# Performance work log

Hardware: AMD Instinct MI355X
Metric: run time of the kernel (lower is better)

Reference implementation:

```python
import jax, jax.numpy as jnp
import numpy as np
import math

D_MODEL = 1024
HEADS = 16
HEAD_DIM = D_MODEL // HEADS
FFN = 4096
B, S = 2, 2048


def _layer_norm(x, gamma, beta, eps=1e-5):
    mean = jnp.mean(x, axis=-1, keepdims=True)
    var = jnp.mean((x - mean) ** 2, axis=-1, keepdims=True)
    return gamma * (x - mean) / jnp.sqrt(var + eps) + beta


def _sdpa(q, k, v, mask):
    # q,k,v: [B,H,S,dh]; mask: [S,S] additive, broadcasts over B,H
    scaled = jnp.einsum('bhqd,bhkd->bhqk', q, k) / math.sqrt(q.shape[-1])
    scaled = scaled + mask
    attn = jax.nn.softmax(scaled, axis=-1)
    return jnp.einsum('bhqk,bhkd->bhqd', attn, v)


def setup_inputs() -> dict:
    key = jax.random.key(0)
    ks = jax.random.split(key, 12)
    s = 0.02
    inp = {
        'x': jax.random.normal(ks[0], (B, S, D_MODEL), jnp.float32),
        'y': jax.random.normal(ks[1], (B, S, D_MODEL), jnp.float32),
        'self_attention_mask': jnp.zeros((S, S), jnp.float32),
        'cross_attention_mask': jnp.zeros((S, S), jnp.float32),
        # self-attention params
        'Wqkv': jax.random.normal(ks[2], (D_MODEL, 3 * D_MODEL), jnp.float32) * s,
        'bqkv': jnp.zeros((3 * D_MODEL,), jnp.float32),
        'Wo1': jax.random.normal(ks[3], (D_MODEL, D_MODEL), jnp.float32) * s,
        'bo1': jnp.zeros((D_MODEL,), jnp.float32),
        # cross-attention params
        'Wkv': jax.random.normal(ks[4], (D_MODEL, 2 * D_MODEL), jnp.float32) * s,
        'bkv': jnp.zeros((2 * D_MODEL,), jnp.float32),
        'Wq': jax.random.normal(ks[5], (D_MODEL, D_MODEL), jnp.float32) * s,
        'bq': jnp.zeros((D_MODEL,), jnp.float32),
        'Wo2': jax.random.normal(ks[6], (D_MODEL, D_MODEL), jnp.float32) * s,
        'bo2': jnp.zeros((D_MODEL,), jnp.float32),
        # layer norms
        'g1': jnp.ones((D_MODEL,), jnp.float32), 'b1': jnp.zeros((D_MODEL,), jnp.float32),
        'g2': jnp.ones((D_MODEL,), jnp.float32), 'b2': jnp.zeros((D_MODEL,), jnp.float32),
        'g3': jnp.ones((D_MODEL,), jnp.float32), 'b3': jnp.zeros((D_MODEL,), jnp.float32),
        # FFN
        'W1': jax.random.normal(ks[7], (D_MODEL, FFN), jnp.float32) * s,
        'bw1': jnp.zeros((FFN,), jnp.float32),
        'W2': jax.random.normal(ks[8], (FFN, D_MODEL), jnp.float32) * s,
        'bw2': jnp.zeros((D_MODEL,), jnp.float32),
    }
    return inp


def reference(x, y, self_attention_mask, cross_attention_mask,
              Wqkv, bqkv, Wo1, bo1, Wkv, bkv, Wq, bq, Wo2, bo2,
              g1, b1, g2, b2, g3, b3, W1, bw1, W2, bw2):
    b, s, d = y.shape

    # ---- masked self-attention on y ----
    qkv = (y @ Wqkv + bqkv).reshape(b, s, HEADS, 3 * HEAD_DIM).transpose(0, 2, 1, 3)
    q, k, v = jnp.split(qkv, 3, axis=-1)  # each [B,H,S,dh]
    vals = _sdpa(q, k, v, self_attention_mask)
    vals = vals.transpose(0, 2, 1, 3).reshape(b, s, d)
    attn_out = vals @ Wo1 + bo1
    # dropout is identity at inference
    y1 = _layer_norm(attn_out + y, g1, b1)

    # ---- cross attention: q from y1, k/v from x ----
    kv = (x @ Wkv + bkv).reshape(b, s, HEADS, 2 * HEAD_DIM).transpose(0, 2, 1, 3)
    k2, v2 = jnp.split(kv, 2, axis=-1)
    q2 = (y1 @ Wq + bq).reshape(b, s, HEADS, HEAD_DIM).transpose(0, 2, 1, 3)
    vals2 = _sdpa(q2, k2, v2, cross_attention_mask)
    vals2 = vals2.transpose(0, 2, 1, 3).reshape(b, s, d)
    cross_out = vals2 @ Wo2 + bo2
    y2 = _layer_norm(cross_out + y1, g2, b2)

    # ---- FFN ----
    h = jax.nn.relu(y2 @ W1 + bw1)
    ffn_out = h @ W2 + bw2
    y3 = _layer_norm(ffn_out + y2, g3, b3)
    return y3
```

## Files before the change

### kernel.cpp

```cpp
#include <hip/hip_runtime.h>
#include <hip/hip_bf16.h>

#define SEQ      2048
#define BATCH    2
#define DMODEL   1024
#define NHEADS   16
#define HDIM     64
#define FFN_DIM  4096
#define MROWS    (BATCH*SEQ)

typedef __attribute__((ext_vector_type(8))) short bf16x8;
typedef __attribute__((ext_vector_type(4))) float f32x4;

#define GFENCE() asm volatile("" ::: "memory")
#define SBAR()   do { GFENCE(); __builtin_amdgcn_s_barrier(); GFENCE(); } while (0)

__device__ __forceinline__ unsigned short f2b(float f) {
    union { float f; unsigned int u; } v; v.f = f;
    unsigned int u = v.u;
    return (unsigned short)((u + 0x7FFFu + ((u >> 16) & 1u)) >> 16);
}
__device__ __forceinline__ float b2f(unsigned short h) {
    union { unsigned int u; float f; } v; v.u = ((unsigned int)h) << 16;
    return v.f;
}
__device__ __forceinline__ void gload_lds16(const void* g, void* l) {
    __builtin_amdgcn_global_load_lds((const __attribute__((address_space(1))) void*)g,
                                     (__attribute__((address_space(3))) void*)l, 16, 0, 0);
}

__device__ __forceinline__ void trans_tile(const float* __restrict__ W,
                                           unsigned short* __restrict__ Wt,
                                           int K, int N, int local) {
    __shared__ float t[32][33];
    const int ntx = N >> 5;
    const int bx = local % ntx, by = local / ntx;
    const int n0 = bx * 32, k0 = by * 32;
    const int tx = threadIdx.x & 31, ty = threadIdx.x >> 5;
#pragma unroll
    for (int i = 0; i < 4; i++)
        t[ty + i * 8][tx] = W[(size_t)(k0 + ty + i * 8) * N + n0 + tx];
    __syncthreads();
#pragma unroll
    for (int i = 0; i < 4; i++) {
        const int n = ty + i * 8;
        Wt[(size_t)(n0 + n) * K + k0 + tx] = f2b(t[tx][n]);
    }
}
__device__ __forceinline__ void cast_blk(const float* __restrict__ in,
                                         unsigned short* __restrict__ out, int local) {
    const int i = (local * 256 + threadIdx.x) * 8;
    float4 a = *(const float4*)(in + i);
    float4 b = *(const float4*)(in + i + 4);
    unsigned short r[8] = {f2b(a.x), f2b(a.y), f2b(a.z), f2b(a.w),
                           f2b(b.x), f2b(b.y), f2b(b.z), f2b(b.w)};
    *(uint4*)(out + i) = *(const uint4*)r;
}

__global__ __launch_bounds__(256) void prep(
    const float* Wqkv, const float* Wo1, const float* Wkv, const float* Wq,
    const float* Wo2, const float* W1, const float* W2,
    const float* x, const float* y,
    unsigned short* pWqkvT, unsigned short* pWo1T, unsigned short* pWkvT,
    unsigned short* pWqT, unsigned short* pWo2T, unsigned short* pW1T,
    unsigned short* pW2T, unsigned short* pxbf, unsigned short* pybf) {
    const int bid = blockIdx.x;
    if      (bid < 3072)  trans_tile(Wqkv, pWqkvT, 1024, 3072, bid);
    else if (bid < 4096)  trans_tile(Wo1,  pWo1T,  1024, 1024, bid - 3072);
    else if (bid < 6144)  trans_tile(Wkv,  pWkvT,  1024, 2048, bid - 4096);
    else if (bid < 7168)  trans_tile(Wq,   pWqT,   1024, 1024, bid - 6144);
    else if (bid < 8192)  trans_tile(Wo2,  pWo2T,  1024, 1024, bid - 7168);
    else if (bid < 12288) trans_tile(W1,   pW1T,   1024, 4096, bid - 8192);
    else if (bid < 16384) trans_tile(W2,   pW2T,   4096, 1024, bid - 12288);
    else if (bid < 18432) cast_blk(x, pxbf, bid - 16384);
    else                  cast_blk(y, pybf, bid - 18432);
}

template <int RELU, int WF32, int WB16>
__global__ __launch_bounds__(256) void gemm_bt(const unsigned short* __restrict__ A,
                                               const unsigned short* __restrict__ Bt,
                                               const float* __restrict__ bias,
                                               float* __restrict__ Cf,
                                               unsigned short* __restrict__ Cb,
                                               int M, int N, int K) {
    __shared__ __align__(16) unsigned short As[128 * 32];
    __shared__ __align__(16) unsigned short Bs[128 * 32];
    const int tid  = threadIdx.x;
    const int lane = tid & 63;
    const int w    = tid >> 6;
    const int m0   = blockIdx.y << 7;
    const int n0   = blockIdx.x << 7;
    const int wr   = (w >> 1) << 6;
    const int wc   = (w & 1) << 6;
    const int srow = lane >> 2;
    const int scol = (lane & 3) << 3;

    f32x4 acc[4][4];
#pragma unroll
    for (int mi = 0; mi < 4; mi++)
#pragma unroll
        for (int ni = 0; ni < 4; ni++) acc[mi][ni] = (f32x4){0.f, 0.f, 0.f, 0.f};

    for (int k0 = 0; k0 < K; k0 += 32) {
#pragma unroll
        for (int t = 0; t < 2; t++) {
            const int rg  = w * 2 + t;
            const int row = (rg << 4) + srow;
            gload_lds16(A  + (size_t)(m0 + row) * K + k0 + scol, (char*)As + (rg << 10));
            gload_lds16(Bt + (size_t)(n0 + row) * K + k0 + scol, (char*)Bs + (rg << 10));
        }
        __syncthreads();
        const int fr = lane & 15;
        const int fk = (lane >> 4) << 3;
        bf16x8 af[4], bfr[4];
#pragma unroll
        for (int i = 0; i < 4; i++) {
            af[i]  = *(const bf16x8*)(As + (wr + (i << 4) + fr) * 32 + fk);
            bfr[i] = *(const bf16x8*)(Bs + (wc + (i << 4) + fr) * 32 + fk);
        }
#pragma unroll
        for (int mi = 0; mi < 4; mi++)
#pragma unroll
            for (int ni = 0; ni < 4; ni++)
                acc[mi][ni] = __builtin_amdgcn_mfma_f32_16x16x32_bf16(af[mi], bfr[ni], acc[mi][ni], 0, 0, 0);
        __syncthreads();
    }

    const int fr = lane & 15;
    const int fq = lane >> 4;
#pragma unroll
    for (int mi = 0; mi < 4; mi++) {
#pragma unroll
        for (int ni = 0; ni < 4; ni++) {
            const int col = n0 + wc + (ni << 4) + fr;
            const float bv = bias[col];
#pragma unroll
            for (int i = 0; i < 4; i++) {
                const int row = m0 + wr + (mi << 4) + (fq << 2) + i;
                float v = acc[mi][ni][i] + bv;
                if (RELU) v = fmaxf(v, 0.f);
                if (WF32) Cf[(size_t)row * N + col] = v;
                if (WB16) Cb[(size_t)row * N + col] = f2b(v);
            }
        }
    }
}

template <int RELU, int WF32, int WB16>
__global__ __launch_bounds__(512, 2) void gemm256(const unsigned short* __restrict__ A,
                                                  const unsigned short* __restrict__ Bt,
                                                  const float* __restrict__ bias,
                                                  float* __restrict__ Cf,
                                                  unsigned short* __restrict__ Cb,
                                                  int M, int N, int K) {
    __shared__ __align__(16) unsigned short lds[2][2][256 * 64];
    const int tid  = threadIdx.x;
    const int lane = tid & 63;
    const int w    = tid >> 6;
    const int q15  = lane & 15;
    const int g    = lane >> 4;
    const int m0   = blockIdx.y << 8;
    const int n0   = blockIdx.x << 8;
    const int wr   = (w >> 2) << 7;
    const int wc   = (w & 3) << 6;

    f32x4 acc[8][4];
#pragma unroll
    for (int m = 0; m < 8; m++)
#pragma unroll
        for (int n = 0; n < 4; n++) acc[m][n] = (f32x4){0.f, 0.f, 0.f, 0.f};

    const int NT = K >> 6;

    auto stage = [&](int which, int buf, int h, int kt, const unsigned short* src, int base0) {
        char* ldsb = (char*)&lds[buf][which][0];
#pragma unroll
        for (int j = 0; j < 2; j++) {
            const int c    = (w << 7) + (j << 6) + lane;
            const int r    = c >> 3, ci = c & 7;
            const int trow = ((r >> 6) << 7) + (h << 6) + (r & 63);
            const int r0   = (w << 4) + (j << 3);
            const int tr0  = ((r0 >> 6) << 7) + (h << 6) + (r0 & 63);
            gload_lds16(src + (size_t)(base0 + trow) * K + (kt << 6) + ((ci ^ (r & 7)) << 3),
                        ldsb + tr0 * 128);
        }
    };
    auto ldA = [&](int buf, int row, int kc) -> bf16x8 {
        return *(const bf16x8*)((const char*)&lds[buf][0][0] + row * 128 + ((kc ^ (row & 7)) << 4));
    };
    auto ldB = [&](int buf, int row, int kc) -> bf16x8 {
        return *(const bf16x8*)((const char*)&lds[buf][1][0] + row * 128 + ((kc ^ (row & 7)) << 4));
    };

    stage(1, 0, 0, 0, Bt, n0);
    stage(1, 0, 1, 0, Bt, n0);
    stage(0, 0, 0, 0, A, m0);
    stage(0, 0, 1, 0, A, m0);

    for (int t = 0; t < NT; ++t) {
        const int buf = t & 1, nb = buf ^ 1;
        const bool st = (t + 1 < NT);
        bf16x8 bfr[4], af[4];

        if (st) { stage(1, nb, 0, t + 1, Bt, n0);
                  asm volatile("s_waitcnt vmcnt(4)" ::: "memory"); }
        else    { asm volatile("s_waitcnt vmcnt(2)" ::: "memory"); }
        SBAR();
#pragma unroll
        for (int n = 0; n < 4; n++) bfr[n] = ldB(buf, wc + n * 16 + q15, g);
#pragma unroll
        for (int m = 0; m < 4; m++) af[m]  = ldA(buf, wr + m * 16 + q15, g);
        __builtin_amdgcn_s_setprio(1);
#pragma unroll
        for (int m = 0; m < 4; m++)
#pragma unroll
            for (int n = 0; n < 4; n++)
                acc[m][n] = __builtin_amdgcn_mfma_f32_16x16x32_bf16(af[m], bfr[n], acc[m][n], 0, 0, 0);
        __builtin_amdgcn_s_setprio(0);
        SBAR();

        if (st) { stage(1, nb, 1, t + 1, Bt, n0);
                  asm volatile("s_waitcnt vmcnt(4)" ::: "memory"); }
        else    { asm volatile("s_waitcnt vmcnt(0)" ::: "memory"); }
        SBAR();
#pragma unroll
        for (int m = 0; m < 4; m++) af[m] = ldA(buf, wr + 64 + m * 16 + q15, g);
        __builtin_amdgcn_s_setprio(1);
#pragma unroll
        for (int m = 0; m < 4; m++)
#pragma unroll
            for (int n = 0; n < 4; n++)
                acc[4 + m][n] = __builtin_amdgcn_mfma_f32_16x16x32_bf16(af[m], bfr[n], acc[4 + m][n], 0, 0, 0);
        __builtin_amdgcn_s_setprio(0);
        SBAR();

        if (st) stage(0, nb, 0, t + 1, A, m0);
        SBAR();
#pragma unroll
        for (int n = 0; n < 4; n++) bfr[n] = ldB(buf, wc + n * 16 + q15, 4 + g);
#pragma unroll
        for (int m = 0; m < 4; m++) af[m]  = ldA(buf, wr + m * 16 + q15, 4 + g);
        __builtin_amdgcn_s_setprio(1);
#pragma unroll
        for (int m = 0; m < 4; m++)
#pragma unroll
            for (int n = 0; n < 4; n++)
                acc[m][n] = __builtin_amdgcn_mfma_f32_16x16x32_bf16(af[m], bfr[n], acc[m][n], 0, 0, 0);
        __builtin_amdgcn_s_setprio(0);
        SBAR();

        if (st) stage(0, nb, 1, t + 1, A, m0);
        SBAR();
#pragma unroll
        for (int m = 0; m < 4; m++) af[m] = ldA(buf, wr + 64 + m * 16 + q15, 4 + g);
        __builtin_amdgcn_s_setprio(1);
#pragma unroll
        for (int m = 0; m < 4; m++)
#pragma unroll
            for (int n = 0; n < 4; n++)
                acc[4 + m][n] = __builtin_amdgcn_mfma_f32_16x16x32_bf16(af[m], bfr[n], acc[4 + m][n], 0, 0, 0);
        __builtin_amdgcn_s_setprio(0);
        SBAR();
    }

#pragma unroll
    for (int mh = 0; mh < 2; mh++)
#pragma unroll
        for (int mf = 0; mf < 4; mf++)
#pragma unroll
            for (int nf = 0; nf < 4; nf++) {
                const int col = n0 + wc + nf * 16 + q15;
                const float bv = bias[col];
#pragma unroll
                for (int i = 0; i < 4; i++) {
                    const int row = m0 + wr + mh * 64 + mf * 16 + (g << 2) + i;
                    float v = acc[mh * 4 + mf][nf][i] + bv;
                    if (RELU) v = fmaxf(v, 0.f);
                    if (WF32) Cf[(size_t)row * N + col] = v;
                    if (WB16) Cb[(size_t)row * N + col] = f2b(v);
                }
            }
}

template <int WB16>
__global__ __launch_bounds__(256) void resid_ln(const float* __restrict__ xin,
                                                const float* __restrict__ res,
                                                const float* __restrict__ g,
                                                const float* __restrict__ b,
                                                float* __restrict__ outf,
                                                unsigned short* __restrict__ outb) {
    const int row = blockIdx.x;
    const int tid = threadIdx.x;
    const size_t base = (size_t)row * 1024 + tid * 4;
    float4 xv = *(const float4*)(xin + base);
    float4 rv = *(const float4*)(res + base);
    const float v0 = xv.x + rv.x, v1 = xv.y + rv.y, v2 = xv.z + rv.z, v3 = xv.w + rv.w;
    float s  = v0 + v1 + v2 + v3;
    float sq = v0 * v0 + v1 * v1 + v2 * v2 + v3 * v3;
#pragma unroll
    for (int off = 32; off; off >>= 1) { s += __shfl_xor(s, off); sq += __shfl_xor(sq, off); }
    __shared__ float red[8];
    if ((tid & 63) == 0) { red[tid >> 6] = s; red[4 + (tid >> 6)] = sq; }
    __syncthreads();
    s  = red[0] + red[1] + red[2] + red[3];
    sq = red[4] + red[5] + red[6] + red[7];
    const float mean = s * (1.0f / 1024.0f);
    const float var  = sq * (1.0f / 1024.0f) - mean * mean;
    const float inv  = rsqrtf(var + 1e-5f);
    const int col = tid * 4;
    float4 gv = *(const float4*)(g + col);
    float4 bv = *(const float4*)(b + col);
    const float o0 = (v0 - mean) * inv * gv.x + bv.x;
    const float o1 = (v1 - mean) * inv * gv.y + bv.y;
    const float o2 = (v2 - mean) * inv * gv.z + bv.z;
    const float o3 = (v3 - mean) * inv * gv.w + bv.w;
    float4 ov = {o0, o1, o2, o3};
    *(float4*)(outf + base) = ov;
    if (WB16) {
        uint2 u;
        u.x = (unsigned int)f2b(o0) | ((unsigned int)f2b(o1) << 16);
        u.y = (unsigned int)f2b(o2) | ((unsigned int)f2b(o3) << 16);
        *(uint2*)(outb + base) = u;
    }
}

__global__ __launch_bounds__(512) void attn_mfma2(
    const unsigned short* __restrict__ Qb, int q_rs, int q_ho,
    const unsigned short* __restrict__ Kb, int k_rs, int k_ho,
    const unsigned short* __restrict__ Vb, int v_rs, int v_ho,
    const float* __restrict__ mask,
    unsigned short* __restrict__ Ob, int o_rs, int o_ho) {
    __shared__ __align__(16) unsigned short Kls[64 * 64];
    __shared__ __align__(16) unsigned short Vraw[64 * 64];
    __shared__ __align__(16) unsigned short QVt[128 * 64];
    __shared__ __align__(16) unsigned short Pls[8][16 * 64];

    const int tid  = threadIdx.x;
    const int lane = tid & 63;
    const int w    = tid >> 6;
    const int g    = lane >> 4;
    const int q15  = lane & 15;
    const int swz  = (lane & 7) << 4;
    const int bh   = blockIdx.y;
    const int b    = bh >> 4, h = bh & 15;
    const int q0   = blockIdx.x << 7;
    const size_t rowbase = (size_t)b * SEQ;

    char* Kc = (char*)Kls;
    char* Vc = (char*)Vraw;
    char* Tc = (char*)QVt;
    char* Pc = (char*)(&Pls[w][0]);

    const int hq = h * q_ho, hk = h * k_ho, hv = h * v_ho;

    auto stage64 = [&](const unsigned short* base, int rs, int hoff, int row0, char* ldsb) {
        const int c = tid;
        const int r = c >> 3, ci = c & 7;
        gload_lds16(base + (rowbase + row0 + r) * (size_t)rs + hoff + ((ci ^ (r & 7)) << 3),
                    ldsb + ((c >> 6) << 10));
    };

#pragma unroll
    for (int bb = 0; bb < 2; bb++) {
        const int c = tid + (bb << 9);
        const int r = c >> 3, ci = c & 7;
        gload_lds16(Qb + (rowbase + q0 + r) * (size_t)q_rs + hq + ((ci ^ (r & 7)) << 3),
                    Tc + ((c >> 6) << 10));
    }
    stage64(Kb, k_rs, hk, 0, Kc);
    stage64(Vb, v_rs, hv, 0, Vc);

    float m_run = -3.0e38f, l_run = 0.f;
    f32x4 oacc[4];
#pragma unroll
    for (int fd = 0; fd < 4; fd++) oacc[fd] = (f32x4){0.f, 0.f, 0.f, 0.f};

    __syncthreads();
    bf16x8 qf[2];
#pragma unroll
    for (int s = 0; s < 2; s++)
        qf[s] = *(const bf16x8*)(Tc + (w * 16 + q15) * 128 + (((s << 6) + (g << 4)) ^ swz));
    __syncthreads();

    const float* mrow_ptr = mask + (size_t)(q0 + w * 16 + q15) * SEQ;

    for (int t = 0; t < 32; t++) {
        const int kv0 = t << 6;
        {
            unsigned short t8[8];
#pragma unroll
            for (int m = 0; m < 8; m++)
                t8[m] = *(const unsigned short*)(Vc + (w * 8 + m) * 128 + ((2 * lane) ^ (m << 4)));
            *(uint4*)(Tc + lane * 128 + ((w << 4) ^ swz)) = *(const uint4*)t8;
        }
        f32x4 sacc[4];
#pragma unroll
        for (int f = 0; f < 4; f++) sacc[f] = (f32x4){0.f, 0.f, 0.f, 0.f};
#pragma unroll
        for (int s = 0; s < 2; s++)
#pragma unroll
            for (int f = 0; f < 4; f++) {
                bf16x8 kf = *(const bf16x8*)(Kc + (f * 16 + q15) * 128 + (((s << 6) + (g << 4)) ^ swz));
                sacc[f] = __builtin_amdgcn_mfma_f32_16x16x32_bf16(kf, qf[s], sacc[f], 0, 0, 0);
            }
        float p[4][4];
        float mt = -3.0e38f;
#pragma unroll
        for (int f = 0; f < 4; f++) {
            float4 mk = *(const float4*)(mrow_ptr + kv0 + f * 16 + g * 4);
            const float* mkp = (const float*)&mk;
#pragma unroll
            for (int r = 0; r < 4; r++) {
                const float v = sacc[f][r] * 0.125f + mkp[r];
                p[f][r] = v;
                mt = fmaxf(mt, v);
            }
        }
        mt = fmaxf(mt, __shfl_xor(mt, 16));
        mt = fmaxf(mt, __shfl_xor(mt, 32));
        bool rescale = !__all(mt <= m_run + 8.0f);
        float alpha = 1.0f;
        if (rescale) {
            const float mnew = fmaxf(m_run, mt);
            alpha = __expf(m_run - mnew);
            m_run = mnew;
        }
        float lsum = 0.f;
#pragma unroll
        for (int f = 0; f < 4; f++)
#pragma unroll
            for (int r = 0; r < 4; r++) {
                const float e = __expf(p[f][r] - m_run);
                p[f][r] = e;
                lsum += e;
            }
        lsum += __shfl_xor(lsum, 16);
        lsum += __shfl_xor(lsum, 32);
        l_run = l_run * alpha + lsum;
#pragma unroll
        for (int f = 0; f < 4; f++) {
            const unsigned int w0 = (unsigned int)f2b(p[f][0]) | ((unsigned int)f2b(p[f][1]) << 16);
            const unsigned int w1 = (unsigned int)f2b(p[f][2]) | ((unsigned int)f2b(p[f][3]) << 16);
            const int bbase = ((f << 5) + (g << 3)) ^ swz;
            *(unsigned int*)(Pc + q15 * 128 + bbase)     = w0;
            *(unsigned int*)(Pc + q15 * 128 + bbase + 4) = w1;
        }
        __syncthreads();
        if (t < 31) {
            stage64(Kb, k_rs, hk, kv0 + 64, Kc);
            stage64(Vb, v_rs, hv, kv0 + 64, Vc);
        }
        if (rescale) {
            float ar[4];
#pragma unroll
            for (int r = 0; r < 4; r++) ar[r] = __shfl(alpha, (g << 4) + (g << 2) + r);
#pragma unroll
            for (int fd = 0; fd < 4; fd++)
#pragma unroll
                for (int r = 0; r < 4; r++) oacc[fd][r] *= ar[r];
        }
#pragma unroll
        for (int s = 0; s < 2; s++) {
            const bf16x8 pf = *(const bf16x8*)(Pc + q15 * 128 + (((s << 6) + (g << 4)) ^ swz));
#pragma unroll
            for (int fd = 0; fd < 4; fd++) {
                const bf16x8 vf = *(const bf16x8*)(Tc + (fd * 16 + q15) * 128 + (((s << 6) + (g << 4)) ^ swz));
                oacc[fd] = __builtin_amdgcn_mfma_f32_16x16x32_bf16(pf, vf, oacc[fd], 0, 0, 0);
            }
        }
        __syncthreads();
    }

    const float rl = 1.0f / l_run;
    float invr[4];
#pragma unroll
    for (int r = 0; r < 4; r++) invr[r] = __shfl(rl, (g << 4) + (g << 2) + r);
    const size_t orow0 = rowbase + q0 + w * 16;
#pragma unroll
    for (int fd = 0; fd < 4; fd++)
#pragma unroll
        for (int r = 0; r < 4; r++) {
            const int qq = (g << 2) + r;
            Ob[(orow0 + qq) * (size_t)o_rs + h * o_ho + fd * 16 + q15] = f2b(oacc[fd][r] * invr[r]);
        }
}

extern "C" void kernel_launch(void* const* d_in, const int* in_sizes, int n_in,
                              void* d_out, int out_size, void* d_ws, size_t ws_size,
                              hipStream_t stream) {
    const float* x     = (const float*)d_in[0];
    const float* y     = (const float*)d_in[1];
    const float* mask1 = (const float*)d_in[2];
    const float* mask2 = (const float*)d_in[3];
    const float* Wqkv  = (const float*)d_in[4];
    const float* bqkv  = (const float*)d_in[5];
    const float* Wo1   = (const float*)d_in[6];
    const float* bo1   = (const float*)d_in[7];
    const float* Wkv   = (const float*)d_in[8];
    const float* bkv   = (const float*)d_in[9];
    const float* Wq    = (const float*)d_in[10];
    const float* bq    = (const float*)d_in[11];
    const float* Wo2   = (const float*)d_in[12];
    const float* bo2   = (const float*)d_in[13];
    const float* g1    = (const float*)d_in[14];
    const float* b1    = (const float*)d_in[15];
    const float* g2    = (const float*)d_in[16];
    const float* b2    = (const float*)d_in[17];
    const float* g3    = (const float*)d_in[18];
    const float* b3    = (const float*)d_in[19];
    const float* W1    = (const float*)d_in[20];
    const float* bw1   = (const float*)d_in[21];
    const float* W2    = (const float*)d_in[22];
    const float* bw2   = (const float*)d_in[23];

    char* ws = (char*)d_ws;
    const size_t o_WqkvT = 0;
    const size_t o_Wo1T  = o_WqkvT + 6291456;
    const size_t o_WkvT  = o_Wo1T  + 2097152;
    const size_t o_WqT   = o_WkvT  + 4194304;
    const size_t o_Wo2T  = o_WqT   + 2097152;
    const size_t o_W1T   = o_Wo2T  + 2097152;
    const size_t o_W2T   = o_W1T   + 8388608;
    const size_t o_xbf   = o_W2T   + 8388608;
    const size_t o_ybf   = o_xbf   + 8388608;
    const size_t o_qkv   = o_ybf   + 8388608;
    const size_t o_vals  = o_qkv   + 25165824;
    const size_t o_tmp   = o_vals  + 8388608;
    const size_t o_y1    = o_tmp   + 16777216;
    const size_t o_y1bf  = o_y1    + 16777216;
    const size_t o_y2    = o_y1bf  + 8388608;
    const size_t o_y2bf  = o_y2    + 16777216;
    const size_t o_kv    = o_qkv;
    const size_t o_q2    = o_qkv + 16777216;
    const size_t o_hbf   = o_xbf;

    unsigned short* pWqkvT = (unsigned short*)(ws + o_WqkvT);
    unsigned short* pWo1T  = (unsigned short*)(ws + o_Wo1T);
    unsigned short* pWkvT  = (unsigned short*)(ws + o_WkvT);
    unsigned short* pWqT   = (unsigned short*)(ws + o_WqT);
    unsigned short* pWo2T  = (unsigned short*)(ws + o_Wo2T);
    unsigned short* pW1T   = (unsigned short*)(ws + o_W1T);
    unsigned short* pW2T   = (unsigned short*)(ws + o_W2T);
    unsigned short* pxbf   = (unsigned short*)(ws + o_xbf);
    unsigned short* pybf   = (unsigned short*)(ws + o_ybf);
    unsigned short* pqkv   = (unsigned short*)(ws + o_qkv);
    unsigned short* pvals  = (unsigned short*)(ws + o_vals);
    float*          ptmp   = (float*)(ws + o_tmp);
    float*          py1    = (float*)(ws + o_y1);
    unsigned short* py1bf  = (unsigned short*)(ws + o_y1bf);
    float*          py2    = (float*)(ws + o_y2);
    unsigned short* py2bf  = (unsigned short*)(ws + o_y2bf);
    unsigned short* pkv    = (unsigned short*)(ws + o_kv);
    unsigned short* pq2    = (unsigned short*)(ws + o_q2);
    unsigned short* phbf   = (unsigned short*)(ws + o_hbf);

    prep<<<dim3(20480), dim3(256), 0, stream>>>(Wqkv, Wo1, Wkv, Wq, Wo2, W1, W2, x, y,
                                                pWqkvT, pWo1T, pWkvT, pWqT, pWo2T,
                                                pW1T, pW2T, pxbf, pybf);

    gemm256<0, 0, 1><<<dim3(3072 / 256, MROWS / 256), dim3(512), 0, stream>>>(
        pybf, pWqkvT, bqkv, nullptr, pqkv, MROWS, 3072, 1024);
    attn_mfma2<<<dim3(SEQ / 128, BATCH * NHEADS), dim3(512), 0, stream>>>(
        pqkv, 3072, 192, pqkv + 64, 3072, 192, pqkv + 128, 3072, 192,
        mask1, pvals, 1024, 64);
    gemm_bt<0, 1, 0><<<dim3(1024 / 128, MROWS / 128), dim3(256), 0, stream>>>(
        pvals, pWo1T, bo1, ptmp, nullptr, MROWS, 1024, 1024);
    resid_ln<1><<<dim3(MROWS), dim3(256), 0, stream>>>(ptmp, y, g1, b1, py1, py1bf);

    gemm256<0, 0, 1><<<dim3(2048 / 256, MROWS / 256), dim3(512), 0, stream>>>(
        pxbf, pWkvT, bkv, nullptr, pkv, MROWS, 2048, 1024);
    gemm_bt<0, 0, 1><<<dim3(1024 / 128, MROWS / 128), dim3(256), 0, stream>>>(
        py1bf, pWqT, bq, nullptr, pq2, MROWS, 1024, 1024);
    attn_mfma2<<<dim3(SEQ / 128, BATCH * NHEADS), dim3(512), 0, stream>>>(
        pq2, 1024, 64, pkv, 2048, 128, pkv + 64, 2048, 128,
        mask2, pvals, 1024, 64);
    gemm_bt<0, 1, 0><<<dim3(1024 / 128, MROWS / 128), dim3(256), 0, stream>>>(
        pvals, pWo2T, bo2, ptmp, nullptr, MROWS, 1024, 1024);
    resid_ln<1><<<dim3(MROWS), dim3(256), 0, stream>>>(ptmp, py1, g2, b2, py2, py2bf);

    gemm256<1, 0, 1><<<dim3(4096 / 256, MROWS / 256), dim3(512), 0, stream>>>(
        py2bf, pW1T, bw1, nullptr, phbf, MROWS, 4096, 1024);
    gemm_bt<0, 1, 0><<<dim3(1024 / 128, MROWS / 128), dim3(256), 0, stream>>>(
        phbf, pW2T, bw2, ptmp, nullptr, MROWS, 1024, 4096);
    resid_ln<0><<<dim3(MROWS), dim3(256), 0, stream>>>(ptmp, py2, g3, b3, (float*)d_out, nullptr);
}
```

Before: 709.2 us.

## Double-buffer attention K/V staging and split-K the FFN down-projection

The attention kernel now double-buffers K, V and the transposed V tile in LDS. It issues the next tile's loads at the top of each iteration, prefetches the mask early, and drops one block barrier per iteration, so global loads overlap compute. The FFN second GEMM (K=4096) switches to a 256x256-tile split-K kernel with four K slices writing fp32 partials. A new layernorm kernel sums those partials with bias and residual. This adds extra partial-sum memory traffic and LDS usage in exchange for more parallelism and overlap.

```diff
diff --git a/kernel.cpp b/kernel.cpp
--- a/kernel.cpp
+++ b/kernel.cpp
@@ -278,6 +278,137 @@
                     if (RELU) v = fmaxf(v, 0.f);
                     if (WF32) Cf[(size_t)row * N + col] = v;
                     if (WB16) Cb[(size_t)row * N + col] = f2b(v);
+                }
+            }
+}
+
+__global__ __launch_bounds__(512, 2) void gemm256sk(const unsigned short* __restrict__ A,
+                                                    const unsigned short* __restrict__ Bt,
+                                                    float* __restrict__ Cpart,
+                                                    int M, int N, int Kstride, int Kc) {
+    __shared__ __align__(16) unsigned short lds[2][2][256 * 64];
+    const int tid  = threadIdx.x;
+    const int lane = tid & 63;
+    const int w    = tid >> 6;
+    const int q15  = lane & 15;
+    const int g    = lane >> 4;
+    const int m0   = blockIdx.y << 8;
+    const int n0   = blockIdx.x << 8;
+    const int wr   = (w >> 2) << 7;
+    const int wc   = (w & 3) << 6;
+    const int koff = blockIdx.z * Kc;
+
+    f32x4 acc[8][4];
+#pragma unroll
+    for (int m = 0; m < 8; m++)
+#pragma unroll
+        for (int n = 0; n < 4; n++) acc[m][n] = (f32x4){0.f, 0.f, 0.f, 0.f};
+
+    const int NT = Kc >> 6;
+
+    auto stage = [&](int which, int buf, int h, int kt, const unsigned short* src, int base0) {
+        char* ldsb = (char*)&lds[buf][which][0];
+#pragma unroll
+        for (int j = 0; j < 2; j++) {
+            const int c    = (w << 7) + (j << 6) + lane;
+            const int r    = c >> 3, ci = c & 7;
+            const int trow = ((r >> 6) << 7) + (h << 6) + (r & 63);
+            const int r0   = (w << 4) + (j << 3);
+            const int tr0  = ((r0 >> 6) << 7) + (h << 6) + (r0 & 63);
+            gload_lds16(src + (size_t)(base0 + trow) * Kstride + koff + (kt << 6) + ((ci ^ (r & 7)) << 3),
+                        ldsb + tr0 * 128);
+        }
+    };
+    auto ldA = [&](int buf, int row, int kc) -> bf16x8 {
+        return *(const bf16x8*)((const char*)&lds[buf][0][0] + row * 128 + ((kc ^ (row & 7)) << 4));
+    };
+    auto ldB = [&](int buf, int row, int kc) -> bf16x8 {
+        return *(const bf16x8*)((const char*)&lds[buf][1][0] + row * 128 + ((kc ^ (row & 7)) << 4));
+    };
+
+    stage(1, 0, 0, 0, Bt, n0);
+    stage(1, 0, 1, 0, Bt, n0);
+    stage(0, 0, 0, 0, A, m0);
+    stage(0, 0, 1, 0, A, m0);
+
+    for (int t = 0; t < NT; ++t) {
+        const int buf = t & 1, nb = buf ^ 1;
+        const bool st = (t + 1 < NT);
+        bf16x8 bfr[4], af[4];
+
+        if (st) { stage(1, nb, 0, t + 1, Bt, n0);
+                  asm volatile("s_waitcnt vmcnt(4)" ::: "memory"); }
+        else    { asm volatile("s_waitcnt vmcnt(2)" ::: "memory"); }
+        SBAR();
+#pragma unroll
+        for (int n = 0; n < 4; n++) bfr[n] = ldB(buf, wc + n * 16 + q15, g);
+#pragma unroll
+        for (int m = 0; m < 4; m++) af[m]  = ldA(buf, wr + m * 16 + q15, g);
+        __builtin_amdgcn_s_setprio(1);
+#pragma unroll
+        for (int m = 0; m < 4; m++)
+#pragma unroll
+            for (int n = 0; n < 4; n++)
+                acc[m][n] = __builtin_amdgcn_mfma_f32_16x16x32_bf16(af[m], bfr[n], acc[m][n], 0, 0, 0);
+        __builtin_amdgcn_s_setprio(0);
+        SBAR();
+
+        if (st) { stage(1, nb, 1, t + 1, Bt, n0);
+                  asm volatile("s_waitcnt vmcnt(4)" ::: "memory"); }
+        else    { asm volatile("s_waitcnt vmcnt(0)" ::: "memory"); }
+        SBAR();
+#pragma unroll
+        for (int m = 0; m < 4; m++) af[m] = ldA(buf, wr + 64 + m * 16 + q15, g);
+        __builtin_amdgcn_s_setprio(1);
+#pragma unroll
+        for (int m = 0; m < 4; m++)
+#pragma unroll
+            for (int n = 0; n < 4; n++)
+                acc[4 + m][n] = __builtin_amdgcn_mfma_f32_16x16x32_bf16(af[m], bfr[n], acc[4 + m][n], 0, 0, 0);
+        __builtin_amdgcn_s_setprio(0);
+        SBAR();
+
+        if (st) stage(0, nb, 0, t + 1, A, m0);
+        SBAR();
+#pragma unroll
+        for (int n = 0; n < 4; n++) bfr[n] = ldB(buf, wc + n * 16 + q15, 4 + g);
+#pragma unroll
+        for (int m = 0; m < 4; m++) af[m]  = ldA(buf, wr + m * 16 + q15, 4 + g);
+        __builtin_amdgcn_s_setprio(1);
+#pragma unroll
+        for (int m = 0; m < 4; m++)
+#pragma unroll
+            for (int n = 0; n < 4; n++)
+                acc[m][n] = __builtin_amdgcn_mfma_f32_16x16x32_bf16(af[m], bfr[n], acc[m][n], 0, 0, 0);
+        __builtin_amdgcn_s_setprio(0);
+        SBAR();
+
+        if (st) stage(0, nb, 1, t + 1, A, m0);
+        SBAR();
+#pragma unroll
+        for (int m = 0; m < 4; m++) af[m] = ldA(buf, wr + 64 + m * 16 + q15, 4 + g);
+        __builtin_amdgcn_s_setprio(1);
+#pragma unroll
+        for (int m = 0; m < 4; m++)
+#pragma unroll
+            for (int n = 0; n < 4; n++)
+                acc[4 + m][n] = __builtin_amdgcn_mfma_f32_16x16x32_bf16(af[m], bfr[n], acc[4 + m][n], 0, 0, 0);
+        __builtin_amdgcn_s_setprio(0);
+        SBAR();
+    }
+
+    float* Cp = Cpart + (size_t)blockIdx.z * M * N;
+#pragma unroll
+    for (int mh = 0; mh < 2; mh++)
+#pragma unroll
+        for (int mf = 0; mf < 4; mf++)
+#pragma unroll
+            for (int nf = 0; nf < 4; nf++) {
+                const int col = n0 + wc + nf * 16 + q15;
+#pragma unroll
+                for (int i = 0; i < 4; i++) {
+                    const int row = m0 + wr + mh * 64 + mf * 16 + (g << 2) + i;
+                    Cp[(size_t)row * N + col] = acc[mh * 4 + mf][nf][i];
                 }
             }
 }
@@ -324,15 +455,55 @@
     }
 }
 
-__global__ __launch_bounds__(512) void attn_mfma2(
+__global__ __launch_bounds__(256) void resid_ln4(const float* __restrict__ part,
+                                                 const float* __restrict__ bias,
+                                                 const float* __restrict__ res,
+                                                 const float* __restrict__ g,
+                                                 const float* __restrict__ b,
+                                                 float* __restrict__ outf) {
+    const int row = blockIdx.x;
+    const int tid = threadIdx.x;
+    const size_t base = (size_t)row * 1024 + tid * 4;
+    const size_t cs = (size_t)MROWS * 1024;
+    float4 a0 = *(const float4*)(part + base);
+    float4 a1 = *(const float4*)(part + cs + base);
+    float4 a2 = *(const float4*)(part + 2 * cs + base);
+    float4 a3 = *(const float4*)(part + 3 * cs + base);
+    float4 rv = *(const float4*)(res + base);
+    float4 bb = *(const float4*)(bias + tid * 4);
+    const float v0 = a0.x + a1.x + a2.x + a3.x + bb.x + rv.x;
+    const float v1 = a0.y + a1.y + a2.y + a3.y + bb.y + rv.y;
+    const float v2 = a0.z + a1.z + a2.z + a3.z + bb.z + rv.z;
+    const float v3 = a0.w + a1.w + a2.w + a3.w + bb.w + rv.w;
+    float s  = v0 + v1 + v2 + v3;
+    float sq = v0 * v0 + v1 * v1 + v2 * v2 + v3 * v3;
+#pragma unroll
+    for (int off = 32; off; off >>= 1) { s += __shfl_xor(s, off); sq += __shfl_xor(sq, off); }
+    __shared__ float red[8];
+    if ((tid & 63) == 0) { red[tid >> 6] = s; red[4 + (tid >> 6)] = sq; }
+    __syncthreads();
+    s  = red[0] + red[1] + red[2] + red[3];
+    sq = red[4] + red[5] + red[6] + red[7];
+    const float mean = s * (1.0f / 1024.0f);
+    const float var  = sq * (1.0f / 1024.0f) - mean * mean;
+    const float inv  = rsqrtf(var + 1e-5f);
+    const int col = tid * 4;
+    float4 gv = *(const float4*)(g + col);
+    float4 bv = *(const float4*)(b + col);
+    float4 ov = {(v0 - mean) * inv * gv.x + bv.x, (v1 - mean) * inv * gv.y + bv.y,
+                 (v2 - mean) * inv * gv.z + bv.z, (v3 - mean) * inv * gv.w + bv.w};
+    *(float4*)(outf + base) = ov;
+}
+
+__global__ __launch_bounds__(512) void attn_mfma3(
     const unsigned short* __restrict__ Qb, int q_rs, int q_ho,
     const unsigned short* __restrict__ Kb, int k_rs, int k_ho,
     const unsigned short* __restrict__ Vb, int v_rs, int v_ho,
     const float* __restrict__ mask,
     unsigned short* __restrict__ Ob, int o_rs, int o_ho) {
-    __shared__ __align__(16) unsigned short Kls[64 * 64];
-    __shared__ __align__(16) unsigned short Vraw[64 * 64];
-    __shared__ __align__(16) unsigned short QVt[128 * 64];
+    __shared__ __align__(16) unsigned short Kls[2][64 * 64];
+    __shared__ __align__(16) unsigned short Vraw[2][64 * 64];
+    __shared__ __align__(16) unsigned short VtQ[2][64 * 64];
     __shared__ __align__(16) unsigned short Pls[8][16 * 64];
 
     const int tid  = threadIdx.x;
@@ -346,9 +517,7 @@
     const int q0   = blockIdx.x << 7;
     const size_t rowbase = (size_t)b * SEQ;
 
-    char* Kc = (char*)Kls;
-    char* Vc = (char*)Vraw;
-    char* Tc = (char*)QVt;
+    char* Tc = (char*)&VtQ[0][0];
     char* Pc = (char*)(&Pls[w][0]);
 
     const int hq = h * q_ho, hk = h * k_ho, hv = h * v_ho;
@@ -367,8 +536,8 @@
         gload_lds16(Qb + (rowbase + q0 + r) * (size_t)q_rs + hq + ((ci ^ (r & 7)) << 3),
                     Tc + ((c >> 6) << 10));
     }
-    stage64(Kb, k_rs, hk, 0, Kc);
-    stage64(Vb, v_rs, hv, 0, Vc);
+    stage64(Kb, k_rs, hk, 0, (char*)&Kls[0][0]);
+    stage64(Vb, v_rs, hv, 0, (char*)&Vraw[0][0]);
 
     float m_run = -3.0e38f, l_run = 0.f;
     f32x4 oacc[4];
@@ -385,13 +554,26 @@
     const float* mrow_ptr = mask + (size_t)(q0 + w * 16 + q15) * SEQ;
 
     for (int t = 0; t < 32; t++) {
+        const int buf = t & 1, nb = buf ^ 1;
         const int kv0 = t << 6;
+        char* Kc  = (char*)&Kls[buf][0];
+        char* Vc  = (char*)&Vraw[buf][0];
+        char* Vtc = (char*)&VtQ[buf][0];
+
+        float4 mk4[4];
+#pragma unroll
+        for (int f = 0; f < 4; f++)
+            mk4[f] = *(const float4*)(mrow_ptr + kv0 + f * 16 + g * 4);
+        if (t < 31) {
+            stage64(Kb, k_rs, hk, kv0 + 64, (char*)&Kls[nb][0]);
+            stage64(Vb, v_rs, hv, kv0 + 64, (char*)&Vraw[nb][0]);
+        }
         {
             unsigned short t8[8];
 #pragma unroll
             for (int m = 0; m < 8; m++)
                 t8[m] = *(const unsigned short*)(Vc + (w * 8 + m) * 128 + ((2 * lane) ^ (m << 4)));
-            *(uint4*)(Tc + lane * 128 + ((w << 4) ^ swz)) = *(const uint4*)t8;
+            *(uint4*)(Vtc + lane * 128 + ((w << 4) ^ swz)) = *(const uint4*)t8;
         }
         f32x4 sacc[4];
 #pragma unroll
@@ -407,8 +589,7 @@
         float mt = -3.0e38f;
 #pragma unroll
         for (int f = 0; f < 4; f++) {
-            float4 mk = *(const float4*)(mrow_ptr + kv0 + f * 16 + g * 4);
-            const float* mkp = (const float*)&mk;
+            const float* mkp = (const float*)&mk4[f];
 #pragma unroll
             for (int r = 0; r < 4; r++) {
                 const float v = sacc[f][r] * 0.125f + mkp[r];
@@ -418,7 +599,7 @@
         }
         mt = fmaxf(mt, __shfl_xor(mt, 16));
         mt = fmaxf(mt, __shfl_xor(mt, 32));
-        bool rescale = !__all(mt <= m_run + 8.0f);
+        const bool rescale = !__all(mt <= m_run + 8.0f);
         float alpha = 1.0f;
         if (rescale) {
             const float mnew = fmaxf(m_run, mt);
@@ -446,10 +627,6 @@
             *(unsigned int*)(Pc + q15 * 128 + bbase + 4) = w1;
         }
         __syncthreads();
-        if (t < 31) {
-            stage64(Kb, k_rs, hk, kv0 + 64, Kc);
-            stage64(Vb, v_rs, hv, kv0 + 64, Vc);
-        }
         if (rescale) {
             float ar[4];
 #pragma unroll
@@ -464,11 +641,10 @@
             const bf16x8 pf = *(const bf16x8*)(Pc + q15 * 128 + (((s << 6) + (g << 4)) ^ swz));
 #pragma unroll
             for (int fd = 0; fd < 4; fd++) {
-                const bf16x8 vf = *(const bf16x8*)(Tc + (fd * 16 + q15) * 128 + (((s << 6) + (g << 4)) ^ swz));
+                const bf16x8 vf = *(const bf16x8*)(Vtc + (fd * 16 + q15) * 128 + (((s << 6) + (g << 4)) ^ swz));
                 oacc[fd] = __builtin_amdgcn_mfma_f32_16x16x32_bf16(pf, vf, oacc[fd], 0, 0, 0);
             }
         }
-        __syncthreads();
     }
 
     const float rl = 1.0f / l_run;
@@ -533,6 +709,7 @@
     const size_t o_kv    = o_qkv;
     const size_t o_q2    = o_qkv + 16777216;
     const size_t o_hbf   = o_xbf;
+    const size_t o_part  = o_qkv;
 
     unsigned short* pWqkvT = (unsigned short*)(ws + o_WqkvT);
     unsigned short* pWo1T  = (unsigned short*)(ws + o_Wo1T);
@@ -553,6 +730,7 @@
     unsigned short* pkv    = (unsigned short*)(ws + o_kv);
     unsigned short* pq2    = (unsigned short*)(ws + o_q2);
     unsigned short* phbf   = (unsigned short*)(ws + o_hbf);
+    float*          pPart  = (float*)(ws + o_part);
 
     prep<<<dim3(20480), dim3(256), 0, stream>>>(Wqkv, Wo1, Wkv, Wq, Wo2, W1, W2, x, y,
                                                 pWqkvT, pWo1T, pWkvT, pWqT, pWo2T,
@@ -560,7 +738,7 @@
 
     gemm256<0, 0, 1><<<dim3(3072 / 256, MROWS / 256), dim3(512), 0, stream>>>(
         pybf, pWqkvT, bqkv, nullptr, pqkv, MROWS, 3072, 1024);
-    attn_mfma2<<<dim3(SEQ / 128, BATCH * NHEADS), dim3(512), 0, stream>>>(
+    attn_mfma3<<<dim3(SEQ / 128, BATCH * NHEADS), dim3(512), 0, stream>>>(
         pqkv, 3072, 192, pqkv + 64, 3072, 192, pqkv + 128, 3072, 192,
         mask1, pvals, 1024, 64);
     gemm_bt<0, 1, 0><<<dim3(1024 / 128, MROWS / 128), dim3(256), 0, stream>>>(
@@ -571,7 +749,7 @@
         pxbf, pWkvT, bkv, nullptr, pkv, MROWS, 2048, 1024);
     gemm_bt<0, 0, 1><<<dim3(1024 / 128, MROWS / 128), dim3(256), 0, stream>>>(
         py1bf, pWqT, bq, nullptr, pq2, MROWS, 1024, 1024);
-    attn_mfma2<<<dim3(SEQ / 128, BATCH * NHEADS), dim3(512), 0, stream>>>(
+    attn_mfma3<<<dim3(SEQ / 128, BATCH * NHEADS), dim3(512), 0, stream>>>(
         pq2, 1024, 64, pkv, 2048, 128, pkv + 64, 2048, 128,
         mask2, pvals, 1024, 64);
     gemm_bt<0, 1, 0><<<dim3(1024 / 128, MROWS / 128), dim3(256), 0, stream>>>(
@@ -580,7 +758,7 @@
 
     gemm256<1, 0, 1><<<dim3(4096 / 256, MROWS / 256), dim3(512), 0, stream>>>(
         py2bf, pW1T, bw1, nullptr, phbf, MROWS, 4096, 1024);
-    gemm_bt<0, 1, 0><<<dim3(1024 / 128, MROWS / 128), dim3(256), 0, stream>>>(
-        phbf, pW2T, bw2, ptmp, nullptr, MROWS, 1024, 4096);
-    resid_ln<0><<<dim3(MROWS), dim3(256), 0, stream>>>(ptmp, py2, g3, b3, (float*)d_out, nullptr);
-}
+    gemm256sk<<<dim3(1024 / 256, MROWS / 256, 4), dim3(512), 0, stream>>>(
+        phbf, pW2T, pPart, MROWS, 1024, 4096, 1024);
+    resid_ln4<<<dim3(MROWS), dim3(256), 0, stream>>>(pPart, bw2, py2, g3, b3, (float*)d_out);
+}
```

Result: faster. 655.3 us (-7.6%).
